# Kernel tuning notes

Measured on AMD Instinct MI355X. Metric: run time of the kernel, lower is better.

Reference implementation:

```python
import jax, jax.numpy as jnp
import numpy as np

NUM_HEADS = 6
HEAD_SIZE = 64
N_EMBD = 384


def setup_inputs() -> dict:
    key = jax.random.key(0)
    ks = jax.random.split(key, 6)
    B, T, C = 4, 2048, N_EMBD
    D = NUM_HEADS * HEAD_SIZE  # 384
    x = jax.random.normal(ks[0], (B, T, C), dtype=jnp.float32)
    scale = 1.0 / np.sqrt(C)
    Wq = jax.random.normal(ks[1], (C, D), dtype=jnp.float32) * scale
    Wk = jax.random.normal(ks[2], (C, D), dtype=jnp.float32) * scale
    Wv = jax.random.normal(ks[3], (C, D), dtype=jnp.float32) * scale
    Wp = jax.random.normal(ks[4], (D, N_EMBD), dtype=jnp.float32) * scale
    bp = jnp.zeros((N_EMBD,), dtype=jnp.float32)
    return {"x": x, "Wq": Wq, "Wk": Wk, "Wv": Wv, "Wp": Wp, "bp": bp}


def reference(x, Wq, Wk, Wv, Wp, bp):
    B, T, C = x.shape
    H, Dh = NUM_HEADS, HEAD_SIZE
    # QKV projections (no bias), split into heads: [B, H, T, Dh]
    q = (x @ Wq).reshape(B, T, H, Dh).transpose(0, 2, 1, 3)
    k = (x @ Wk).reshape(B, T, H, Dh).transpose(0, 2, 1, 3)
    v = (x @ Wv).reshape(B, T, H, Dh).transpose(0, 2, 1, 3)
    # scaled dot-product scores [B, H, T, T]
    scores = jnp.einsum("bhqd,bhkd->bhqk", q, k) / jnp.sqrt(jnp.float32(Dh))
    causal = jnp.tril(jnp.ones((T, T), dtype=bool))
    scores = jnp.where(causal, scores, jnp.float32(-1e9))
    attn = jax.nn.softmax(scores, axis=-1)
    # dropout is identity at inference (Keras Dropout inactive outside training)
    out = jnp.einsum("bhqk,bhkd->bhqd", attn, v)
    out = out.transpose(0, 2, 1, 3).reshape(B, T, H * Dh)
    return out @ Wp + bp
```

## Files before the change

kernel.cpp:

```cpp
#include <hip/hip_runtime.h>
#include <hip/hip_bf16.h>

typedef __bf16 bf16x8 __attribute__((ext_vector_type(8)));
typedef float floatx4 __attribute__((ext_vector_type(4)));
typedef unsigned short us4 __attribute__((ext_vector_type(4)));
typedef unsigned short us8 __attribute__((ext_vector_type(8)));
typedef unsigned short ushort_t;

#define MFMA(a,b,c) __builtin_amdgcn_mfma_f32_16x16x32_bf16((a),(b),(c),0,0,0)


__device__ __forceinline__ ushort_t f2bf(float f){
  unsigned u = __builtin_bit_cast(unsigned, f);
  u = u + 0x7fffu + ((u>>16)&1u);
  return (ushort_t)(u>>16);
}

__device__ __forceinline__ us4 pack4(float4 a){
  us4 o;
  o[0]=f2bf(a.x); o[1]=f2bf(a.y); o[2]=f2bf(a.z); o[3]=f2bf(a.w);
  return o;
}

__device__ __forceinline__ us4 cvt4(floatx4 v){
  union { us4 s; __hip_bfloat162 h[2]; } u;
  float2 t;
  t.x=v[0]; t.y=v[1]; u.h[0]=__float22bfloat162_rn(t);
  t.x=v[2]; t.y=v[3]; u.h[1]=__float22bfloat162_rn(t);
  return u.s;
}

__global__ __launch_bounds__(256) void prep(
    const float* __restrict__ x,
    const float* __restrict__ w0, const float* __restrict__ w1,
    const float* __restrict__ w2, const float* __restrict__ w3,
    ushort_t* __restrict__ xb,
    ushort_t* __restrict__ wt_qkv, ushort_t* __restrict__ wt_p){
  __shared__ ushort_t tile[64][65];
  int bx = blockIdx.x;
  if (bx < 3072){
    int i = (bx*256 + threadIdx.x)*4;
    int row = i/384, col = i - row*384;
    float4 v = *(const float4*)(x + i);
    us4 o;
    o[0]=f2bf(v.x); o[1]=f2bf(v.y); o[2]=f2bf(v.z); o[3]=f2bf(v.w);
    *(us4*)(xb + ((row>>4)*48 + (col>>3))*128 + (row&15)*8 + (col&7)) = o;
    return;
  }
  int t6 = bx - 3072;
  int z = t6/36, rem = t6%36, by = rem/6, bxx = rem%6;
  const float* src; ushort_t* dst;
  if      (z==0){ src=w0; dst=wt_qkv;             }
  else if (z==1){ src=w1; dst=wt_qkv + 147456;    }
  else if (z==2){ src=w2; dst=wt_qkv + 2*147456;  }
  else          { src=w3; dst=wt_p;               }
  int r0 = by*64, c0 = bxx*64;
  int t = threadIdx.x, r = t>>2, cs = (t&3)*16;
  #pragma unroll
  for (int i=0;i<16;i++) tile[r][cs+i] = f2bf(src[(r0+r)*384 + c0+cs+i]);
  __syncthreads();
  int n = c0 + r, t16n = n>>4, rn = n&15;
  int k0 = r0 + cs;
  #pragma unroll
  for (int i=0;i<16;i++){
    int k = k0 + i;
    dst[(t16n*48 + (k>>3))*128 + rn*8 + (k&7)] = tile[cs+i][r];
  }
}

__global__ __launch_bounds__(64) void qkv_gemm(
    const ushort_t* __restrict__ x, const ushort_t* __restrict__ wt,
    ushort_t* __restrict__ qb, ushort_t* __restrict__ kb, ushort_t* __restrict__ vtb){
  __shared__ ushort_t tr[16*72];
  int lane = threadIdx.x&63, l15 = lane&15, quad = lane>>4;
  int mb = blockIdx.x*64, mt = blockIdx.x*4;
  int z  = blockIdx.y/6;
  int nt16 = (blockIdx.y - z*6)*4;
  int n0 = nt16*16;
  const ushort_t* wbase = wt + z*147456;
  floatx4 acc[4][4];
  #pragma unroll
  for (int qs=0;qs<4;qs++)
    #pragma unroll
    for (int nt=0;nt<4;nt++) acc[qs][nt]=(floatx4){0,0,0,0};
  #pragma unroll
  for (int kt=0; kt<12; kt++){
    bf16x8 a[4], b[4];
    #pragma unroll
    for (int qs=0; qs<4; qs++)
      a[qs] = *(const bf16x8*)(x + ((mt+qs)*48 + kt*4+quad)*128 + l15*8);
    #pragma unroll
    for (int nt=0; nt<4; nt++)
      b[nt] = *(const bf16x8*)(wbase + ((nt16+nt)*48 + kt*4+quad)*128 + l15*8);
    #pragma unroll
    for (int qs=0; qs<4; qs++)
      #pragma unroll
      for (int nt=0; nt<4; nt++)
        acc[qs][nt] = MFMA(a[qs], b[nt], acc[qs][nt]);
  }
  int h = n0>>6;
  if (z == 2){
    #pragma unroll
    for (int qs=0; qs<4; qs++){
      int rbase = mb + qs*16 + quad*4;
      int b_ = rbase >> 11, rr = rbase & 2047;
      int ct = rr>>3, e0 = rr&7;
      #pragma unroll
      for (int nt=0; nt<4; nt++){
        float4 v; v.x=acc[qs][nt][0]; v.y=acc[qs][nt][1];
                  v.z=acc[qs][nt][2]; v.w=acc[qs][nt][3];
        *(us4*)(vtb + ((b_*6+h)*1024 + nt*256 + ct)*128 + l15*8 + e0) = pack4(v);
      }
    }
  } else {
    float qscale = (z==0) ? 0.18033688011112042f : 1.0f;
    ushort_t* dstp = (z==0) ? qb : kb;
    #pragma unroll
    for (int qs=0; qs<4; qs++){
      int rbase = mb + qs*16;
      int b_ = rbase>>11, t16 = (rbase&2047)>>4;
      #pragma unroll
      for (int nt=0; nt<4; nt++)
        #pragma unroll
        for (int j=0; j<4; j++)
          tr[(quad*4+j)*72 + nt*16 + l15] = f2bf(acc[qs][nt][j]*qscale);
      us8 v0 = *(const us8*)(&tr[l15*72 + quad*8]);
      us8 v1 = *(const us8*)(&tr[l15*72 + (quad+4)*8]);
      int hbase = (b_*6+h)*1024 + t16*8;
      *(us8*)(dstp + (hbase + quad  )*128 + l15*8) = v0;
      *(us8*)(dstp + (hbase + quad+4)*128 + l15*8) = v1;
    }
  }
}

__device__ __forceinline__ void score(
    const bf16x8 (&kf)[4][2], bf16x8 qf0, bf16x8 qf1,
    ushort_t* slice, int qg, int kv0, bool diag, int l15, int quad){
  floatx4 s[4];
  #pragma unroll
  for (int nt=0; nt<4; nt++){
    floatx4 z = {0,0,0,0};
    z = MFMA(kf[nt][0], qf0, z);
    z = MFMA(kf[nt][1], qf1, z);
    s[nt] = z;
  }
  ushort_t* prow = slice + l15*72;
  if (diag){
    #pragma unroll
    for (int nt=0; nt<4; nt++){
      floatx4 p;
      #pragma unroll
      for (int r=0;r<4;r++){
        int kvg = kv0 + nt*16 + quad*4 + r;
        float sv = (kvg > qg) ? -1e30f : s[nt][r];
        p[r] = exp2f(sv);
      }
      *(us4*)(prow + nt*16 + quad*4) = cvt4(p);
    }
  } else {
    #pragma unroll
    for (int nt=0; nt<4; nt++){
      floatx4 p;
      #pragma unroll
      for (int r=0;r<4;r++) p[r] = exp2f(s[nt][r]);
      *(us4*)(prow + nt*16 + quad*4) = cvt4(p);
    }
  }
}

__device__ __forceinline__ void pv(
    const bf16x8 (&vf)[4][2], bf16x8 ones, ushort_t* slice,
    floatx4 (&o4)[4], floatx4& lsum, int l15, int quad){
  ushort_t* prow = slice + l15*72;
  bf16x8 pa0 = *(const bf16x8*)(prow + quad*8);
  bf16x8 pa1 = *(const bf16x8*)(prow + 32 + quad*8);
  #pragma unroll
  for (int nt=0; nt<4; nt++){
    o4[nt] = MFMA(pa0, vf[nt][0], o4[nt]);
    o4[nt] = MFMA(pa1, vf[nt][1], o4[nt]);
  }
  lsum = MFMA(pa0, ones, lsum);
  lsum = MFMA(pa1, ones, lsum);
}

__global__ __launch_bounds__(256,2) void attn(
    const ushort_t* __restrict__ qb, const ushort_t* __restrict__ kb,
    const ushort_t* __restrict__ vtb, ushort_t* __restrict__ ob){
  __shared__ float smem[4736];
  int bx = blockIdx.x;
  int hb = bx % 24;
  int ti = bx / 24;
  int t  = 63 - ti;
  int ktm = t >> 1;
  int h = hb % 6, b = hb / 6;
  int lane = threadIdx.x&63, w = threadIdx.x>>6, l15 = lane&15, quad = lane>>4;
  const ushort_t* qbase = qb  + (b*6+h)*131072;
  const ushort_t* kbase = kb  + (b*6+h)*131072;
  const ushort_t* vbase = vtb + (b*6+h)*131072;

  bf16x8 qf[2][2];
  #pragma unroll
  for (int s=0; s<2; s++){
    const ushort_t* qp = qbase + ((t*2+s)*8 + quad)*128 + l15*8;
    qf[s][0] = *(const bf16x8*)(qp);
    qf[s][1] = *(const bf16x8*)(qp + 512);
  }
  union { us8 u; bf16x8 v; } onesu;
  #pragma unroll
  for (int i=0;i<8;i++) onesu.u[i] = 0x3F80;
  bf16x8 ones = onesu.v;

  floatx4 o[2][4];
  floatx4 ls[2];
  #pragma unroll
  for (int s=0;s<2;s++){
    ls[s] = (floatx4){0,0,0,0};
    #pragma unroll
    for (int i=0;i<4;i++) o[s][i]=(floatx4){0,0,0,0};
  }

  ushort_t* s0 = (ushort_t*)smem + w*2304;
  ushort_t* s1 = s0 + 1152;
  int q0 = t*32;

  bf16x8 kf[4][2], vf[4][2];
  for (int kt=w; kt<=ktm; kt+=4){
    int kv0 = kt*64;
    #pragma unroll
    for (int nt=0; nt<4; nt++){
      const ushort_t* kp = kbase + ((kt*4+nt)*8 + quad)*128 + l15*8;
      kf[nt][0] = *(const bf16x8*)(kp);
      kf[nt][1] = *(const bf16x8*)(kp + 512);
      const ushort_t* vp = vbase + (nt*256 + kt*8 + quad)*128 + l15*8;
      vf[nt][0] = *(const bf16x8*)(vp);
      vf[nt][1] = *(const bf16x8*)(vp + 512);
    }
    bool diag = (kt == ktm);
    score(kf, qf[0][0],qf[0][1], s0, q0   +l15, kv0, diag, l15, quad);
    score(kf, qf[1][0],qf[1][1], s1, q0+16+l15, kv0, diag, l15, quad);
    pv(vf, ones, s0, o[0], ls[0], l15, quad);
    pv(vf, ones, s1, o[1], ls[1], l15, quad);
  }

  float* lsh = smem + 4608;
  if (l15==0){
    #pragma unroll
    for (int j=0;j<4;j++){
      lsh[w*32 +      quad*4 + j] = ls[0][j];
      lsh[w*32 + 16 + quad*4 + j] = ls[1][j];
    }
  }

  auto do_chunk = [&](const floatx4 (&oc)[4], int c, int grc){
    __syncthreads();
    #pragma unroll
    for (int j=0;j<4;j++){
      int r16 = quad*4 + j;
      #pragma unroll
      for (int nt=0;nt<4;nt++)
        smem[w*1088 + r16*68 + nt*16 + l15] = oc[nt][j];
    }
    __syncthreads();
    #pragma unroll
    for (int jj=0;jj<4;jj++){
      int r16 = w*4 + jj;
      float l = lsh[c*16+r16] + lsh[32+c*16+r16]
              + lsh[64+c*16+r16] + lsh[96+c*16+r16];
      float acc = smem[r16*68+lane] + smem[1088 + r16*68+lane]
                + smem[2176 + r16*68+lane] + smem[3264 + r16*68+lane];
      ob[((b*128 + grc)*48 + h*8 + (lane>>3))*128 + r16*8 + (lane&7)]
          = f2bf(acc/l);
    }
  };
  do_chunk(o[0], 0, t*2);
  do_chunk(o[1], 1, t*2+1);
}

__global__ __launch_bounds__(64) void proj_gemm(
    const ushort_t* __restrict__ a, const ushort_t* __restrict__ wpt,
    const float* __restrict__ bp, float* __restrict__ out){
  int lane = threadIdx.x&63, l15 = lane&15, quad = lane>>4;
  int mb = blockIdx.x*64, mt = blockIdx.x*4;
  int nb = blockIdx.y*64, nt16 = blockIdx.y*4;
  floatx4 acc[4][4];
  #pragma unroll
  for (int qs=0;qs<4;qs++)
    #pragma unroll
    for (int nt=0;nt<4;nt++) acc[qs][nt]=(floatx4){0,0,0,0};
  #pragma unroll
  for (int kt=0; kt<12; kt++){
    bf16x8 av[4], bv[4];
    #pragma unroll
    for (int qs=0; qs<4; qs++)
      av[qs] = *(const bf16x8*)(a + ((mt+qs)*48 + kt*4+quad)*128 + l15*8);
    #pragma unroll
    for (int nt=0; nt<4; nt++)
      bv[nt] = *(const bf16x8*)(wpt + ((nt16+nt)*48 + kt*4+quad)*128 + l15*8);
    #pragma unroll
    for (int qs=0; qs<4; qs++)
      #pragma unroll
      for (int nt=0; nt<4; nt++)
        acc[qs][nt] = MFMA(av[qs], bv[nt], acc[qs][nt]);
  }
  #pragma unroll
  for (int qs=0; qs<4; qs++){
    #pragma unroll
    for (int nt=0; nt<4; nt++){
      int c = nb + nt*16 + l15;
      float bias = bp[c];
      #pragma unroll
      for (int j=0; j<4; j++){
        int r = mb + qs*16 + quad*4 + j;
        out[r*384 + c] = acc[qs][nt][j] + bias;
      }
    }
  }
}

extern "C" void kernel_launch(void* const* d_in, const int* in_sizes, int n_in,
                              void* d_out, int out_size, void* d_ws, size_t ws_size,
                              hipStream_t stream){
  const float* x  = (const float*)d_in[0];
  const float* Wq = (const float*)d_in[1];
  const float* Wk = (const float*)d_in[2];
  const float* Wv = (const float*)d_in[3];
  const float* Wp = (const float*)d_in[4];
  const float* bp = (const float*)d_in[5];
  float* out = (float*)d_out;

  ushort_t* xb  = (ushort_t*)d_ws;
  ushort_t* wt  = xb  + 8192*384;
  ushort_t* wpt = wt  + 1152*384;
  ushort_t* qb  = wpt + 384*384;
  ushort_t* kb  = qb  + 8192*384;
  ushort_t* vtb = kb  + 8192*384;
  ushort_t* ab  = vtb + 8192*384;

  prep     <<<dim3(3216),   256, 0, stream>>>(x,Wq,Wk,Wv,Wp,xb,wt,wpt);
  qkv_gemm <<<dim3(128,18), 64,  0, stream>>>(xb, wt, qb, kb, vtb);
  attn     <<<dim3(1536),   256, 0, stream>>>(qb, kb, vtb, ab);
  proj_gemm<<<dim3(128,6),  64,  0, stream>>>(ab, wpt, bp, out);
}
```

Before: 131.9 us.

## Split attention by query tiles per wave instead of KV split across waves

Result: slower. 141.2 us (+7.0%).

```diff
diff --git a/kernel.cpp b/kernel.cpp
--- a/kernel.cpp
+++ b/kernel.cpp
@@ -133,99 +133,42 @@
   }
 }
 
-__device__ __forceinline__ void score(
-    const bf16x8 (&kf)[4][2], bf16x8 qf0, bf16x8 qf1,
-    ushort_t* slice, int qg, int kv0, bool diag, int l15, int quad){
-  floatx4 s[4];
-  #pragma unroll
-  for (int nt=0; nt<4; nt++){
-    floatx4 z = {0,0,0,0};
-    z = MFMA(kf[nt][0], qf0, z);
-    z = MFMA(kf[nt][1], qf1, z);
-    s[nt] = z;
-  }
-  ushort_t* prow = slice + l15*72;
-  if (diag){
-    #pragma unroll
-    for (int nt=0; nt<4; nt++){
-      floatx4 p;
-      #pragma unroll
-      for (int r=0;r<4;r++){
-        int kvg = kv0 + nt*16 + quad*4 + r;
-        float sv = (kvg > qg) ? -1e30f : s[nt][r];
-        p[r] = exp2f(sv);
-      }
-      *(us4*)(prow + nt*16 + quad*4) = cvt4(p);
-    }
-  } else {
-    #pragma unroll
-    for (int nt=0; nt<4; nt++){
-      floatx4 p;
-      #pragma unroll
-      for (int r=0;r<4;r++) p[r] = exp2f(s[nt][r]);
-      *(us4*)(prow + nt*16 + quad*4) = cvt4(p);
-    }
-  }
-}
-
-__device__ __forceinline__ void pv(
-    const bf16x8 (&vf)[4][2], bf16x8 ones, ushort_t* slice,
-    floatx4 (&o4)[4], floatx4& lsum, int l15, int quad){
-  ushort_t* prow = slice + l15*72;
-  bf16x8 pa0 = *(const bf16x8*)(prow + quad*8);
-  bf16x8 pa1 = *(const bf16x8*)(prow + 32 + quad*8);
-  #pragma unroll
-  for (int nt=0; nt<4; nt++){
-    o4[nt] = MFMA(pa0, vf[nt][0], o4[nt]);
-    o4[nt] = MFMA(pa1, vf[nt][1], o4[nt]);
-  }
-  lsum = MFMA(pa0, ones, lsum);
-  lsum = MFMA(pa1, ones, lsum);
-}
-
-__global__ __launch_bounds__(256,2) void attn(
+__global__ __launch_bounds__(256,3) void attn(
     const ushort_t* __restrict__ qb, const ushort_t* __restrict__ kb,
     const ushort_t* __restrict__ vtb, ushort_t* __restrict__ ob){
-  __shared__ float smem[4736];
+  __shared__ ushort_t smem[4608];
   int bx = blockIdx.x;
   int hb = bx % 24;
-  int ti = bx / 24;
-  int t  = 63 - ti;
-  int ktm = t >> 1;
+  int blk = 31 - bx/24;
   int h = hb % 6, b = hb / 6;
   int lane = threadIdx.x&63, w = threadIdx.x>>6, l15 = lane&15, quad = lane>>4;
+  int tau = blk*4 + w;
+  int ktm = blk;
   const ushort_t* qbase = qb  + (b*6+h)*131072;
   const ushort_t* kbase = kb  + (b*6+h)*131072;
   const ushort_t* vbase = vtb + (b*6+h)*131072;
 
-  bf16x8 qf[2][2];
-  #pragma unroll
-  for (int s=0; s<2; s++){
-    const ushort_t* qp = qbase + ((t*2+s)*8 + quad)*128 + l15*8;
-    qf[s][0] = *(const bf16x8*)(qp);
-    qf[s][1] = *(const bf16x8*)(qp + 512);
-  }
+  bf16x8 qf0, qf1;
+  { const ushort_t* qp = qbase + (tau*8 + quad)*128 + l15*8;
+    qf0 = *(const bf16x8*)(qp);
+    qf1 = *(const bf16x8*)(qp + 512); }
   union { us8 u; bf16x8 v; } onesu;
   #pragma unroll
   for (int i=0;i<8;i++) onesu.u[i] = 0x3F80;
   bf16x8 ones = onesu.v;
 
-  floatx4 o[2][4];
-  floatx4 ls[2];
-  #pragma unroll
-  for (int s=0;s<2;s++){
-    ls[s] = (floatx4){0,0,0,0};
-    #pragma unroll
-    for (int i=0;i<4;i++) o[s][i]=(floatx4){0,0,0,0};
-  }
-
-  ushort_t* s0 = (ushort_t*)smem + w*2304;
-  ushort_t* s1 = s0 + 1152;
-  int q0 = t*32;
-
-  bf16x8 kf[4][2], vf[4][2];
-  for (int kt=w; kt<=ktm; kt+=4){
+  floatx4 o[4];
+  floatx4 ls = (floatx4){0,0,0,0};
+  #pragma unroll
+  for (int i=0;i<4;i++) o[i]=(floatx4){0,0,0,0};
+
+  ushort_t* slice = smem + w*1152;
+  ushort_t* prow  = slice + l15*72;
+  int qg = tau*16 + l15;
+
+  for (int kt=0; kt<=ktm; ++kt){
     int kv0 = kt*64;
+    bf16x8 kf[4][2], vf[4][2];
     #pragma unroll
     for (int nt=0; nt<4; nt++){
       const ushort_t* kp = kbase + ((kt*4+nt)*8 + quad)*128 + l15*8;
@@ -235,45 +178,56 @@
       vf[nt][0] = *(const bf16x8*)(vp);
       vf[nt][1] = *(const bf16x8*)(vp + 512);
     }
-    bool diag = (kt == ktm);
-    score(kf, qf[0][0],qf[0][1], s0, q0   +l15, kv0, diag, l15, quad);
-    score(kf, qf[1][0],qf[1][1], s1, q0+16+l15, kv0, diag, l15, quad);
-    pv(vf, ones, s0, o[0], ls[0], l15, quad);
-    pv(vf, ones, s1, o[1], ls[1], l15, quad);
-  }
-
-  float* lsh = smem + 4608;
-  if (l15==0){
-    #pragma unroll
-    for (int j=0;j<4;j++){
-      lsh[w*32 +      quad*4 + j] = ls[0][j];
-      lsh[w*32 + 16 + quad*4 + j] = ls[1][j];
-    }
-  }
-
-  auto do_chunk = [&](const floatx4 (&oc)[4], int c, int grc){
-    __syncthreads();
-    #pragma unroll
-    for (int j=0;j<4;j++){
-      int r16 = quad*4 + j;
-      #pragma unroll
-      for (int nt=0;nt<4;nt++)
-        smem[w*1088 + r16*68 + nt*16 + l15] = oc[nt][j];
-    }
-    __syncthreads();
-    #pragma unroll
-    for (int jj=0;jj<4;jj++){
-      int r16 = w*4 + jj;
-      float l = lsh[c*16+r16] + lsh[32+c*16+r16]
-              + lsh[64+c*16+r16] + lsh[96+c*16+r16];
-      float acc = smem[r16*68+lane] + smem[1088 + r16*68+lane]
-                + smem[2176 + r16*68+lane] + smem[3264 + r16*68+lane];
-      ob[((b*128 + grc)*48 + h*8 + (lane>>3))*128 + r16*8 + (lane&7)]
-          = f2bf(acc/l);
-    }
-  };
-  do_chunk(o[0], 0, t*2);
-  do_chunk(o[1], 1, t*2+1);
+    floatx4 s[4];
+    #pragma unroll
+    for (int nt=0; nt<4; nt++){
+      floatx4 z = {0,0,0,0};
+      z = MFMA(kf[nt][0], qf0, z);
+      z = MFMA(kf[nt][1], qf1, z);
+      s[nt] = z;
+    }
+    if (kt == ktm){
+      #pragma unroll
+      for (int nt=0; nt<4; nt++){
+        floatx4 p;
+        #pragma unroll
+        for (int r=0;r<4;r++){
+          int kvg = kv0 + nt*16 + quad*4 + r;
+          float sv = (kvg > qg) ? -1e30f : s[nt][r];
+          p[r] = exp2f(sv);
+        }
+        *(us4*)(prow + nt*16 + quad*4) = cvt4(p);
+      }
+    } else {
+      #pragma unroll
+      for (int nt=0; nt<4; nt++){
+        floatx4 p;
+        #pragma unroll
+        for (int r=0;r<4;r++) p[r] = exp2f(s[nt][r]);
+        *(us4*)(prow + nt*16 + quad*4) = cvt4(p);
+      }
+    }
+    bf16x8 pa0 = *(const bf16x8*)(prow + quad*8);
+    bf16x8 pa1 = *(const bf16x8*)(prow + 32 + quad*8);
+    #pragma unroll
+    for (int nt=0; nt<4; nt++){
+      o[nt] = MFMA(pa0, vf[nt][0], o[nt]);
+      o[nt] = MFMA(pa1, vf[nt][1], o[nt]);
+    }
+    ls = MFMA(pa0, ones, ls);
+    ls = MFMA(pa1, ones, ls);
+  }
+
+  #pragma unroll
+  for (int nt=0; nt<4; nt++)
+    #pragma unroll
+    for (int j=0; j<4; j++)
+      slice[(quad*4+j)*72 + nt*16 + l15] = f2bf(o[nt][j] / ls[j]);
+  us8 v0 = *(const us8*)(&slice[l15*72 + quad*8]);
+  us8 v1 = *(const us8*)(&slice[l15*72 + (quad+4)*8]);
+  int base = (b*128 + tau)*48 + h*8;
+  *(us8*)(ob + (base + quad  )*128 + l15*8) = v0;
+  *(us8*)(ob + (base + quad+4)*128 + l15*8) = v1;
 }
 
 __global__ __launch_bounds__(64) void proj_gemm(
@@ -338,6 +292,6 @@
 
   prep     <<<dim3(3216),   256, 0, stream>>>(x,Wq,Wk,Wv,Wp,xb,wt,wpt);
   qkv_gemm <<<dim3(128,18), 64,  0, stream>>>(xb, wt, qb, kb, vtb);
-  attn     <<<dim3(1536),   256, 0, stream>>>(qb, kb, vtb, ab);
+  attn     <<<dim3(768),    256, 0, stream>>>(qb, kb, vtb, ab);
   proj_gemm<<<dim3(128,6),  64,  0, stream>>>(ab, wpt, bp, out);
 }
```
